# Optimization experiments

Measured on AMD Instinct MI355X. Metric: run time of the kernel, lower is better.

## Reference

```python
import jax, jax.numpy as jnp
import numpy as np

N, E, D_IN, D_AGG, D_OUT = 40000, 640000, 128, 128, 64


def setup_inputs() -> dict:
    key = jax.random.key(0)
    ks = jax.random.split(key, 16)

    def lin(kw, fan_in, fan_out):
        s = 1.0 / np.sqrt(fan_in)
        return jax.random.uniform(kw, (fan_in, fan_out), jnp.float32, -s, s)

    return {
        "x_self": jax.random.normal(ks[0], (N, D_IN), jnp.float32),
        "x_neighbor": jax.random.normal(ks[1], (N, D_AGG), jnp.float32),
        "edge_index": jax.random.randint(ks[2], (2, E), 0, N, jnp.int64),
        # linear_in_self: D_IN -> 2*D_OUT
        "W_in_self": lin(ks[3], D_IN, 2 * D_OUT),
        "b_in_self": jnp.zeros((2 * D_OUT,), jnp.float32),
        # linear_out_self: D_IN + 2*D_OUT -> D_OUT
        "W_out_self": lin(ks[4], D_IN + 2 * D_OUT, D_OUT),
        "b_out_self": jnp.zeros((D_OUT,), jnp.float32),
        # gcn1: D_IN -> 2*D_OUT ; gcn2: 2*D_OUT -> D_OUT
        "Wg1": lin(ks[5], D_IN, 2 * D_OUT),
        "bg1": jnp.zeros((2 * D_OUT,), jnp.float32),
        "Wg2": lin(ks[6], 2 * D_OUT, D_OUT),
        "bg2": jnp.zeros((D_OUT,), jnp.float32),
        # linear_out: D_AGG + D_OUT -> D_OUT
        "W_out": lin(ks[7], D_AGG + D_OUT, D_OUT),
        "b_out": jnp.zeros((D_OUT,), jnp.float32),
    }


def _gcn(x, W, b, row, col, norm, n):
    # PyG GCNConv: linear transform, then normalized gather/scatter-add
    h = x @ W                              # [N, out]
    msg = h[row] * norm[:, None]           # [E+N, out] gathered messages
    return jax.ops.segment_sum(msg, col, num_segments=n) + b


def reference(x_self, x_neighbor, edge_index,
              W_in_self, b_in_self, W_out_self, b_out_self,
              Wg1, bg1, Wg2, bg2, W_out, b_out):
    n = x_self.shape[0]
    loop = jnp.arange(n, dtype=edge_index.dtype)
    row = jnp.concatenate([edge_index[0], loop])   # sources (+ self-loops)
    col = jnp.concatenate([edge_index[1], loop])   # targets (+ self-loops)
    deg = jax.ops.segment_sum(jnp.ones_like(col, jnp.float32), col, num_segments=n)
    dis = jnp.where(deg > 0, jax.lax.rsqrt(jnp.maximum(deg, 1.0)), 0.0)
    norm = dis[row] * dis[col]

    # self branch
    l1 = jax.nn.relu(x_self @ W_in_self + b_in_self)
    l1 = jnp.concatenate([x_self, l1], axis=1)
    l1 = l1 @ W_out_self + b_out_self

    # GCN aggregation branch (no activation between convs, per source)
    g1 = _gcn(x_self, Wg1, bg1, row, col, norm, n)
    g2 = _gcn(g1, Wg2, bg2, row, col, norm, n)
    x2 = jnp.concatenate([x_neighbor, g2], axis=1) @ W_out + b_out
    return (l1, x2)
```

## Files before the change

### kernel.cpp

```cpp
#include <hip/hip_runtime.h>
#include <hip/hip_fp16.h>

typedef short s8v __attribute__((ext_vector_type(8)));
typedef float f4v __attribute__((ext_vector_type(4)));
typedef unsigned short u16x8 __attribute__((ext_vector_type(8)));

__device__ __forceinline__ unsigned short f2bf(float f) {
  unsigned u = __float_as_uint(f);
  u = (u + 0x7fffu + ((u >> 16) & 1u)) >> 16;
  return (unsigned short)u;
}
__device__ __forceinline__ float bf2f(unsigned short s) {
  return __uint_as_float(((unsigned)s) << 16);
}

__device__ __forceinline__ void pack_one(const float* __restrict__ W,
                                         unsigned short* __restrict__ P,
                                         int NCf, int stride, int t) {
  const int lane = t & 63;
  const int ct = (t >> 6) % (NCf / 16);
  const int kc = (t >> 6) / (NCf / 16);
  const int col = ct * 16 + (lane & 15);
  const int krow = kc * 32 + (lane >> 4) * 8;
  unsigned short tmp[8];
#pragma unroll
  for (int j = 0; j < 8; ++j) tmp[j] = f2bf(W[(krow + j) * stride + col]);
  uint4 o;
  o.x = (unsigned)tmp[0] | ((unsigned)tmp[1] << 16);
  o.y = (unsigned)tmp[2] | ((unsigned)tmp[3] << 16);
  o.z = (unsigned)tmp[4] | ((unsigned)tmp[5] << 16);
  o.w = (unsigned)tmp[6] | ((unsigned)tmp[7] << 16);
  reinterpret_cast<uint4*>(P)[t] = o;
}

__global__ __launch_bounds__(256) void prep_kernel(
    const float* __restrict__ x, unsigned short* __restrict__ S1,
    int* __restrict__ deg, const float* __restrict__ Wis,
    const float* __restrict__ Wos, const float* __restrict__ Wo,
    unsigned short* __restrict__ P, int cvtB, int zeroB, int N) {
  const int blk = blockIdx.x;
  const int tid = threadIdx.x;
  if (blk < cvtB) {
    const int i = blk * 256 + tid;
    const float4 v = reinterpret_cast<const float4*>(x)[i];
    ushort4 o;
    o.x = f2bf(v.x); o.y = f2bf(v.y); o.z = f2bf(v.z); o.w = f2bf(v.w);
    reinterpret_cast<ushort4*>(S1)[i] = o;
    return;
  }
  const int b1 = blk - cvtB;
  if (b1 < zeroB) {
    const int i = b1 * 256 + tid;
    if (i < N) deg[i] = 0;
    return;
  }
  const int b = b1 - zeroB;
  if (b < 4)        pack_one(Wis,            P + 0,     64, 128, b * 256 + tid);
  else if (b < 8)   pack_one(Wis + 64,       P + 8192,  64, 128, (b - 4) * 256 + tid);
  else if (b < 12)  pack_one(Wos,            P + 16384, 64, 64,  (b - 8) * 256 + tid);
  else if (b < 16)  pack_one(Wos + 128 * 64, P + 24576, 64, 64,  (b - 12) * 256 + tid);
  else if (b < 20)  pack_one(Wo,             P + 32768, 64, 64,  (b - 16) * 256 + tid);
  else              pack_one(Wo + 128 * 64,  P + 40960, 64, 64,  (b - 20) * 256 + tid);
}

__global__ __launch_bounds__(256) void deg_w12_kernel(
    const int* __restrict__ cols, int* __restrict__ deg, int E, int degB,
    const float* __restrict__ Wg1, const float* __restrict__ Wg2,
    const float* __restrict__ bg1, unsigned short* __restrict__ P12,
    float* __restrict__ bvec) {
  const int blk = blockIdx.x;
  if (blk < degB) {
    const int i = blk * 256 + threadIdx.x;
    if (i < E) atomicAdd(&deg[cols[i]], 1);
    return;
  }
  const int b = blk - degB;
  if (b < 32) {
    const int t = b * 256 + threadIdx.x;
    const int i = t >> 6, j = t & 63;
    float acc = 0.f;
    for (int k = 0; k < 128; ++k)
      acc = fmaf(Wg1[i * 128 + k], Wg2[k * 64 + j], acc);
    const int kc = i >> 5;
    const int lane = ((i >> 3) & 3) * 16 + (j & 15);
    const int jj = i & 7;
    const int ct = j >> 4;
    P12[((kc * 4 + ct) * 64 + lane) * 8 + jj] = f2bf(acc);
  } else if (threadIdx.x < 64) {
    const int j = threadIdx.x;
    float acc = 0.f;
    for (int k = 0; k < 128; ++k) acc = fmaf(bg1[k], Wg2[k * 64 + j], acc);
    bvec[j] = acc;
  }
}

__device__ __forceinline__ void stage16k(unsigned short* __restrict__ Bs,
                                         const unsigned short* __restrict__ src) {
  uint4* d = reinterpret_cast<uint4*>(Bs);
  const uint4* s = reinterpret_cast<const uint4*>(src);
  for (int i = threadIdx.x; i < 1024; i += 256) d[i] = s[i];
}

__device__ __forceinline__ void load_a_bf16(s8v a[4],
                                            const unsigned short* __restrict__ A,
                                            int arow, int koff) {
#pragma unroll
  for (int kc = 0; kc < 4; ++kc)
    a[kc] = *reinterpret_cast<const s8v*>(A + (long long)arow * 128 + kc * 32 + koff);
}

__device__ __forceinline__ void load_a_f32(s8v a[4],
                                           const float* __restrict__ A,
                                           int arow, int koff) {
#pragma unroll
  for (int kc = 0; kc < 4; ++kc) {
    const float4 f0 = *reinterpret_cast<const float4*>(
        A + (long long)arow * 128 + kc * 32 + koff);
    const float4 f1 = *reinterpret_cast<const float4*>(
        A + (long long)arow * 128 + kc * 32 + koff + 4);
    s8v r;
    r[0] = (short)f2bf(f0.x); r[1] = (short)f2bf(f0.y);
    r[2] = (short)f2bf(f0.z); r[3] = (short)f2bf(f0.w);
    r[4] = (short)f2bf(f1.x); r[5] = (short)f2bf(f1.y);
    r[6] = (short)f2bf(f1.z); r[7] = (short)f2bf(f1.w);
    a[kc] = r;
  }
}

__device__ __forceinline__ void mfma_panel(f4v acc[4], const s8v a[4],
                                           const unsigned short* __restrict__ Bs,
                                           int lane) {
#pragma unroll
  for (int kc = 0; kc < 4; ++kc)
#pragma unroll
    for (int ct = 0; ct < 4; ++ct) {
      const s8v b =
          *reinterpret_cast<const s8v*>(&Bs[((kc * 4 + ct) * 64 + lane) * 8]);
      acc[ct] = __builtin_amdgcn_mfma_f32_16x16x32_bf16(a[kc], b, acc[ct], 0, 0, 0);
    }
}

__device__ __forceinline__ void gemm1_body(
    unsigned short* __restrict__ Bs, const unsigned short* __restrict__ S1,
    const unsigned short* __restrict__ P, const float* __restrict__ bis,
    unsigned short* __restrict__ S2h, int blk) {
  const int tid = threadIdx.x;
  const int wave = tid >> 6, lane = tid & 63;
  const int row0 = blk * 64 + wave * 16;
  const int arow = row0 + (lane & 15);
  const int koff = (lane >> 4) * 8;
  s8v a1[4];
  load_a_bf16(a1, S1, arow, koff);
  f4v acc[8] = {};
#pragma unroll
  for (int h = 0; h < 2; ++h) {
    if (h) __syncthreads();
    stage16k(Bs, P + h * 8192);
    __syncthreads();
    mfma_panel(&acc[h * 4], a1, Bs, lane);
  }
  const int crow0 = row0 + (lane >> 4) * 4;
  const int ccol = lane & 15;
#pragma unroll
  for (int h = 0; h < 2; ++h)
#pragma unroll
    for (int ctl = 0; ctl < 4; ++ctl) {
      const int col = h * 64 + ctl * 16 + ccol;
      const float bv = bis[col];
#pragma unroll
      for (int r = 0; r < 4; ++r) {
        const float v = fmaxf(acc[h * 4 + ctl][r] + bv, 0.f);
        S2h[(long long)(crow0 + r) * 128 + col] = f2bf(v);
      }
    }
}

__device__ __forceinline__ void gemm2_body(
    unsigned short* __restrict__ Bs, const unsigned short* __restrict__ S1,
    const unsigned short* __restrict__ S2h, const unsigned short* __restrict__ P0,
    const unsigned short* __restrict__ P1, const float* __restrict__ bos,
    float* __restrict__ out1, int blk) {
  const int tid = threadIdx.x;
  const int wave = tid >> 6, lane = tid & 63;
  const int row0 = blk * 64 + wave * 16;
  const int arow = row0 + (lane & 15);
  const int koff = (lane >> 4) * 8;
  s8v a1[4], a2[4];
  load_a_bf16(a1, S1, arow, koff);
  load_a_bf16(a2, S2h, arow, koff);
  f4v acc[4] = {};
  stage16k(Bs, P0);
  __syncthreads();
  mfma_panel(acc, a1, Bs, lane);
  __syncthreads();
  stage16k(Bs, P1);
  __syncthreads();
  mfma_panel(acc, a2, Bs, lane);
  const int crow0 = row0 + (lane >> 4) * 4;
  const int ccol = lane & 15;
#pragma unroll
  for (int ct = 0; ct < 4; ++ct) {
    const int col = ct * 16 + ccol;
    const float bv = bos[col];
#pragma unroll
    for (int r = 0; r < 4; ++r)
      out1[(long long)(crow0 + r) * 64 + col] = acc[ct][r] + bv;
  }
}

template <int K1, bool OUT_BF16, bool A1F32, bool ACCUM>
__device__ __forceinline__ void gemm64_body(
    unsigned short* __restrict__ Bs, const void* __restrict__ A1v,
    const unsigned short* __restrict__ P1, const float* __restrict__ bias,
    void* __restrict__ Cout, int blk) {
  constexpr int KC1 = K1 / 32;
  const int tid = threadIdx.x;
  {
    uint4* d = reinterpret_cast<uint4*>(Bs);
    const uint4* s = reinterpret_cast<const uint4*>(P1);
    constexpr int n1 = K1 * 64 / 8;
    for (int i = tid; i < n1; i += 256) d[i] = s[i];
  }
  const int wave = tid >> 6, lane = tid & 63;
  const int row0 = blk * 64 + wave * 16;
  const int arow = row0 + (lane & 15);
  const int koff = (lane >> 4) * 8;
  s8v a1[KC1];
  if constexpr (A1F32) {
    const float* A1f = (const float*)A1v;
#pragma unroll
    for (int kc = 0; kc < KC1; ++kc) {
      const float4 f0 = *reinterpret_cast<const float4*>(
          A1f + (long long)arow * K1 + kc * 32 + koff);
      const float4 f1 = *reinterpret_cast<const float4*>(
          A1f + (long long)arow * K1 + kc * 32 + koff + 4);
      s8v r;
      r[0] = (short)f2bf(f0.x); r[1] = (short)f2bf(f0.y);
      r[2] = (short)f2bf(f0.z); r[3] = (short)f2bf(f0.w);
      r[4] = (short)f2bf(f1.x); r[5] = (short)f2bf(f1.y);
      r[6] = (short)f2bf(f1.z); r[7] = (short)f2bf(f1.w);
      a1[kc] = r;
    }
  } else {
    const unsigned short* A1b = (const unsigned short*)A1v;
#pragma unroll
    for (int kc = 0; kc < KC1; ++kc)
      a1[kc] = *reinterpret_cast<const s8v*>(A1b + (long long)arow * K1 +
                                             kc * 32 + koff);
  }
  __syncthreads();
  f4v acc[4] = {};
#pragma unroll
  for (int kc = 0; kc < KC1; ++kc)
#pragma unroll
    for (int ct = 0; ct < 4; ++ct) {
      const s8v b =
          *reinterpret_cast<const s8v*>(&Bs[((kc * 4 + ct) * 64 + lane) * 8]);
      acc[ct] = __builtin_amdgcn_mfma_f32_16x16x32_bf16(a1[kc], b, acc[ct], 0, 0, 0);
    }
  const int crow0 = row0 + (lane >> 4) * 4;
  const int ccol = lane & 15;
#pragma unroll
  for (int ct = 0; ct < 4; ++ct) {
    const int col = ct * 16 + ccol;
    const float bv = bias ? bias[col] : 0.f;
#pragma unroll
    for (int r = 0; r < 4; ++r) {
      const long long idx = (long long)(crow0 + r) * 64 + col;
      float v = acc[ct][r] + bv;
      if (ACCUM) v += ((float*)Cout)[idx];
      if (OUT_BF16)
        ((unsigned short*)Cout)[idx] = f2bf(v);
      else
        ((float*)Cout)[idx] = v;
    }
  }
}

template <bool PASS_B>
__device__ __forceinline__ void gather_body(
    const unsigned short* __restrict__ h, const unsigned* __restrict__ csr,
    const int* __restrict__ off, const float* __restrict__ dis,
    float* __restrict__ s_out, const float* __restrict__ s_in,
    const float* __restrict__ bvec, const float* __restrict__ bias,
    unsigned short* __restrict__ out, int N, int gb, int nblk) {
  const int wid = (gb * 256 + (int)threadIdx.x) >> 6;
  const int lane = threadIdx.x & 63;
  const int grp = lane >> 3;
  const int sl = lane & 7;
  const int stride = nblk * 32;

  float bb[8], bv[8];
  if constexpr (PASS_B) {
    const float4 b0 = *reinterpret_cast<const float4*>(bias + sl * 8);
    const float4 b1 = *reinterpret_cast<const float4*>(bias + sl * 8 + 4);
    bb[0] = b0.x; bb[1] = b0.y; bb[2] = b0.z; bb[3] = b0.w;
    bb[4] = b1.x; bb[5] = b1.y; bb[6] = b1.z; bb[7] = b1.w;
    const float4 v0 = *reinterpret_cast<const float4*>(bvec + sl * 8);
    const float4 v1 = *reinterpret_cast<const float4*>(bvec + sl * 8 + 4);
    bv[0] = v0.x; bv[1] = v0.y; bv[2] = v0.z; bv[3] = v0.w;
    bv[4] = v1.x; bv[5] = v1.y; bv[6] = v1.z; bv[7] = v1.w;
  }

  for (int n = wid * 8 + grp; n < N; n += stride) {
    const float dn = dis[n];
    const float dn2 = dn * dn;
    float a[8];
    {
      const u16x8 hv =
          *reinterpret_cast<const u16x8*>(h + (long long)n * 64 + sl * 8);
#pragma unroll
      for (int q = 0; q < 8; ++q) a[q] = bf2f(hv[q]) * dn2;
    }
    float sw = dn2;
    const int start = (n == 0) ? 0 : off[n - 1];
    const int end = off[n];
    int j = start;
    for (; j + 3 < end; j += 4) {
      const unsigned e0 = csr[j], e1 = csr[j + 1];
      const unsigned e2 = csr[j + 2], e3 = csr[j + 3];
      const u16x8 u0 = *reinterpret_cast<const u16x8*>(
          h + (long long)(e0 & 0xffffu) * 64 + sl * 8);
      const u16x8 u1 = *reinterpret_cast<const u16x8*>(
          h + (long long)(e1 & 0xffffu) * 64 + sl * 8);
      const u16x8 u2 = *reinterpret_cast<const u16x8*>(
          h + (long long)(e2 & 0xffffu) * 64 + sl * 8);
      const u16x8 u3 = *reinterpret_cast<const u16x8*>(
          h + (long long)(e3 & 0xffffu) * 64 + sl * 8);
      const float w0 = __half2float(__ushort_as_half((unsigned short)(e0 >> 16)));
      const float w1 = __half2float(__ushort_as_half((unsigned short)(e1 >> 16)));
      const float w2 = __half2float(__ushort_as_half((unsigned short)(e2 >> 16)));
      const float w3 = __half2float(__ushort_as_half((unsigned short)(e3 >> 16)));
#pragma unroll
      for (int q = 0; q < 8; ++q) {
        a[q] = fmaf(bf2f(u0[q]), w0, a[q]);
        a[q] = fmaf(bf2f(u1[q]), w1, a[q]);
        a[q] = fmaf(bf2f(u2[q]), w2, a[q]);
        a[q] = fmaf(bf2f(u3[q]), w3, a[q]);
      }
      if constexpr (!PASS_B) sw += (w0 + w1) + (w2 + w3);
    }
    for (; j < end; ++j) {
      const unsigned e = csr[j];
      const u16x8 u = *reinterpret_cast<const u16x8*>(
          h + (long long)(e & 0xffffu) * 64 + sl * 8);
      const float w = __half2float(__ushort_as_half((unsigned short)(e >> 16)));
#pragma unroll
      for (int q = 0; q < 8; ++q) a[q] = fmaf(bf2f(u[q]), w, a[q]);
      if constexpr (!PASS_B) sw += w;
    }
    u16x8 o;
    if constexpr (!PASS_B) {
      if (sl == 0) s_out[n] = sw;
#pragma unroll
      for (int q = 0; q < 8; ++q) o[q] = f2bf(a[q]);
    } else {
      const float si = s_in[n];
#pragma unroll
      for (int q = 0; q < 8; ++q) o[q] = f2bf(fmaf(si, bv[q], a[q] + bb[q]));
    }
    *reinterpret_cast<u16x8*>(out + (long long)n * 64 + sl * 8) = o;
  }
}

__global__ __launch_bounds__(1024) void scan1_kernel(
    const int* __restrict__ deg, int* __restrict__ off, int* __restrict__ part,
    float* __restrict__ dis, int N) {
  __shared__ int s[1024];
  const int tid = threadIdx.x;
  const int i = blockIdx.x * 1024 + tid;
  const int v = (i < N) ? deg[i] : 0;
  if (i < N) dis[i] = rsqrtf((float)v + 1.0f);
  s[tid] = v;
  __syncthreads();
  for (int o = 1; o < 1024; o <<= 1) {
    const int t = (tid >= o) ? s[tid - o] : 0;
    __syncthreads();
    s[tid] += t;
    __syncthreads();
  }
  if (i < N) off[i] = s[tid] - v;
  if (tid == 1023) part[blockIdx.x] = s[1023];
}

__global__ __launch_bounds__(1024) void scan3_kernel(
    int* __restrict__ off, const int* __restrict__ part, int N) {
  __shared__ int pp;
  if (threadIdx.x < 64) {
    int v = (threadIdx.x < blockIdx.x) ? part[threadIdx.x] : 0;
#pragma unroll
    for (int o = 32; o > 0; o >>= 1) v += __shfl_down(v, o, 64);
    if (threadIdx.x == 0) pp = v;
  }
  __syncthreads();
  const int i = blockIdx.x * 1024 + threadIdx.x;
  if (i < N) off[i] += pp;
}

__global__ __launch_bounds__(256) void mega_kernel(
    const unsigned short* __restrict__ S1, const float* __restrict__ x_nb,
    const unsigned short* __restrict__ P, const float* __restrict__ bis,
    const float* __restrict__ bo, unsigned short* __restrict__ S2h,
    unsigned short* __restrict__ S4, float* __restrict__ out2,
    const int* __restrict__ rows, const int* __restrict__ cols,
    int* __restrict__ off, const float* __restrict__ dis,
    unsigned* __restrict__ csr, int E, int GB) {
  __shared__ unsigned short Bs[8192];
  const int b = blockIdx.x;
  if (b < GB) {
    gemm1_body(Bs, S1, P, bis, S2h, b);
  } else if (b < 2 * GB) {
    gemm64_body<128, true, false, false>(Bs, S1, P + 45056, nullptr, S4, b - GB);
  } else if (b < 3 * GB) {
    gemm64_body<128, false, true, false>(Bs, x_nb, P + 32768, bo, out2, b - 2 * GB);
  } else {
    const int i = (b - 3 * GB) * 256 + (int)threadIdx.x;
    if (i < E) {
      const int c = cols[i];
      const int r = rows[i];
      const int pos = atomicAdd(&off[c], 1);
      const unsigned wb = __half_as_ushort(__float2half(dis[r] * dis[c]));
      csr[pos] = (wb << 16) | (unsigned)r;
    }
  }
}

__global__ __launch_bounds__(256) void g2ga_kernel(
    const unsigned short* __restrict__ S1, const unsigned short* __restrict__ S2h,
    const unsigned short* __restrict__ P, const float* __restrict__ bos,
    float* __restrict__ out1, const unsigned short* __restrict__ S4,
    const unsigned* __restrict__ csr, const int* __restrict__ off,
    const float* __restrict__ dis, float* __restrict__ s_out,
    unsigned short* __restrict__ S3, int N, int GB, int GGB) {
  __shared__ unsigned short Bs[8192];
  const int b = blockIdx.x;
  if (b < GB) {
    gemm2_body(Bs, S1, S2h, P + 16384, P + 24576, bos, out1, b);
  } else {
    gather_body<false>(S4, csr, off, dis, s_out, nullptr, nullptr, nullptr, S3,
                       N, b - GB, GGB);
  }
}

__global__ __launch_bounds__(256) void gatherB_kernel(
    const unsigned short* __restrict__ S3, const unsigned* __restrict__ csr,
    const int* __restrict__ off, const float* __restrict__ dis,
    const float* __restrict__ s_in, const float* __restrict__ bvec,
    const float* __restrict__ bias, unsigned short* __restrict__ G2, int N) {
  gather_body<true>(S3, csr, off, dis, nullptr, s_in, bvec, bias, G2, N,
                    blockIdx.x, gridDim.x);
}

__global__ __launch_bounds__(256) void g4b_kernel(
    const unsigned short* __restrict__ G2, const unsigned short* __restrict__ P,
    float* __restrict__ out2) {
  __shared__ unsigned short Bs[4096];
  gemm64_body<64, false, false, true>(Bs, G2, P + 40960, nullptr, out2,
                                      blockIdx.x);
}

extern "C" void kernel_launch(void* const* d_in, const int* in_sizes, int n_in,
                              void* d_out, int out_size, void* d_ws,
                              size_t ws_size, hipStream_t stream) {
  const float* x_self = (const float*)d_in[0];
  const float* x_nb = (const float*)d_in[1];
  const int* ei = (const int*)d_in[2];
  const float* Wis = (const float*)d_in[3];
  const float* bis = (const float*)d_in[4];
  const float* Wos = (const float*)d_in[5];
  const float* bos = (const float*)d_in[6];
  const float* Wg1 = (const float*)d_in[7];
  const float* bg1 = (const float*)d_in[8];
  const float* Wg2 = (const float*)d_in[9];
  const float* bg2 = (const float*)d_in[10];
  const float* Wo = (const float*)d_in[11];
  const float* bo = (const float*)d_in[12];

  const int N = in_sizes[0] / 128;
  const int E = (int)(in_sizes[2] / 2);
  const int* rows = ei;
  const int* cols = ei + E;

  float* out1 = (float*)d_out;
  float* out2 = out1 + (long long)N * 64;

  float* dis = (float*)d_ws;
  int* deg = (int*)(dis + N);
  int* off = deg + N;
  int* part = off + N + 16;
  float* s = (float*)(part + 64);
  float* bvec = s + N;
  unsigned* csr = (unsigned*)(bvec + 64);
  unsigned short* S1 = (unsigned short*)(csr + E);
  unsigned short* S2h = S1 + (long long)N * 128;
  unsigned short* S3 = S2h + (long long)N * 128;
  unsigned short* S4 = S3 + (long long)N * 64;
  unsigned short* P = S4 + (long long)N * 64;
  unsigned short* pW12 = P + 45056;

  const int NB = (N + 1023) / 1024;
  const int GB = N / 64;
  const int GGB = (N + 31) / 32;

  const int cvtB = (N * 32 + 255) / 256;
  const int zeroB = (N + 255) / 256;
  const int degB = (E + 255) / 256;

  prep_kernel<<<cvtB + zeroB + 22, 256, 0, stream>>>(
      x_self, S1, deg, Wis, Wos, Wo, P, cvtB, zeroB, N);
  deg_w12_kernel<<<degB + 33, 256, 0, stream>>>(cols, deg, E, degB, Wg1, Wg2,
                                                bg1, pW12, bvec);
  scan1_kernel<<<NB, 1024, 0, stream>>>(deg, off, part, dis, N);
  scan3_kernel<<<NB, 1024, 0, stream>>>(off, part, N);
  mega_kernel<<<3 * GB + degB, 256, 0, stream>>>(
      S1, x_nb, P, bis, bo, S2h, S4, out2, rows, cols, off, dis, csr, E, GB);
  g2ga_kernel<<<GB + GGB, 256, 0, stream>>>(S1, S2h, P, bos, out1, S4, csr,
                                            off, dis, s, S3, N, GB, GGB);
  gatherB_kernel<<<GGB, 256, 0, stream>>>(S3, csr, off, dis, s, bvec, bg2, S1, N);
  g4b_kernel<<<GB, 256, 0, stream>>>(S1, P, out2);
}
```

Baseline: 130.3 us.

## Fuse final 64x64 output GEMM into second gather and reorder block dispatch

The separate g4b GEMM kernel is removed: the second GCN gather now multiplies each aggregated 64-wide row by the W_out slice held in shared memory (fp32, using lane shuffles) and accumulates into out2 directly. This drops one launch and a bf16 round trip of the G2 intermediate. In exchange, the gather kernel does per-row scalar FMA work in place of MFMA. Block ordering in mega_kernel and g2ga_kernel is also swapped so the CSR-fill and gather blocks are dispatched before the GEMM blocks, which should help the latency-bound work start early.

```diff
diff --git a/kernel.cpp b/kernel.cpp
--- a/kernel.cpp
+++ b/kernel.cpp
@@ -59,8 +59,7 @@
   else if (b < 8)   pack_one(Wis + 64,       P + 8192,  64, 128, (b - 4) * 256 + tid);
   else if (b < 12)  pack_one(Wos,            P + 16384, 64, 64,  (b - 8) * 256 + tid);
   else if (b < 16)  pack_one(Wos + 128 * 64, P + 24576, 64, 64,  (b - 12) * 256 + tid);
-  else if (b < 20)  pack_one(Wo,             P + 32768, 64, 64,  (b - 16) * 256 + tid);
-  else              pack_one(Wo + 128 * 64,  P + 40960, 64, 64,  (b - 20) * 256 + tid);
+  else              pack_one(Wo,             P + 32768, 64, 64,  (b - 16) * 256 + tid);
 }
 
 __global__ __launch_bounds__(256) void deg_w12_kernel(
@@ -109,24 +108,6 @@
     a[kc] = *reinterpret_cast<const s8v*>(A + (long long)arow * 128 + kc * 32 + koff);
 }
 
-__device__ __forceinline__ void load_a_f32(s8v a[4],
-                                           const float* __restrict__ A,
-                                           int arow, int koff) {
-#pragma unroll
-  for (int kc = 0; kc < 4; ++kc) {
-    const float4 f0 = *reinterpret_cast<const float4*>(
-        A + (long long)arow * 128 + kc * 32 + koff);
-    const float4 f1 = *reinterpret_cast<const float4*>(
-        A + (long long)arow * 128 + kc * 32 + koff + 4);
-    s8v r;
-    r[0] = (short)f2bf(f0.x); r[1] = (short)f2bf(f0.y);
-    r[2] = (short)f2bf(f0.z); r[3] = (short)f2bf(f0.w);
-    r[4] = (short)f2bf(f1.x); r[5] = (short)f2bf(f1.y);
-    r[6] = (short)f2bf(f1.z); r[7] = (short)f2bf(f1.w);
-    a[kc] = r;
-  }
-}
-
 __device__ __forceinline__ void mfma_panel(f4v acc[4], const s8v a[4],
                                            const unsigned short* __restrict__ Bs,
                                            int lane) {
@@ -208,32 +189,30 @@
   }
 }
 
-template <int K1, bool OUT_BF16, bool A1F32, bool ACCUM>
+template <bool OUT_BF16, bool A1F32>
 __device__ __forceinline__ void gemm64_body(
     unsigned short* __restrict__ Bs, const void* __restrict__ A1v,
     const unsigned short* __restrict__ P1, const float* __restrict__ bias,
     void* __restrict__ Cout, int blk) {
-  constexpr int KC1 = K1 / 32;
   const int tid = threadIdx.x;
   {
     uint4* d = reinterpret_cast<uint4*>(Bs);
     const uint4* s = reinterpret_cast<const uint4*>(P1);
-    constexpr int n1 = K1 * 64 / 8;
-    for (int i = tid; i < n1; i += 256) d[i] = s[i];
+    for (int i = tid; i < 1024; i += 256) d[i] = s[i];
   }
   const int wave = tid >> 6, lane = tid & 63;
   const int row0 = blk * 64 + wave * 16;
   const int arow = row0 + (lane & 15);
   const int koff = (lane >> 4) * 8;
-  s8v a1[KC1];
+  s8v a1[4];
   if constexpr (A1F32) {
     const float* A1f = (const float*)A1v;
 #pragma unroll
-    for (int kc = 0; kc < KC1; ++kc) {
+    for (int kc = 0; kc < 4; ++kc) {
       const float4 f0 = *reinterpret_cast<const float4*>(
-          A1f + (long long)arow * K1 + kc * 32 + koff);
+          A1f + (long long)arow * 128 + kc * 32 + koff);
       const float4 f1 = *reinterpret_cast<const float4*>(
-          A1f + (long long)arow * K1 + kc * 32 + koff + 4);
+          A1f + (long long)arow * 128 + kc * 32 + koff + 4);
       s8v r;
       r[0] = (short)f2bf(f0.x); r[1] = (short)f2bf(f0.y);
       r[2] = (short)f2bf(f0.z); r[3] = (short)f2bf(f0.w);
@@ -242,22 +221,11 @@
       a1[kc] = r;
     }
   } else {
-    const unsigned short* A1b = (const unsigned short*)A1v;
-#pragma unroll
-    for (int kc = 0; kc < KC1; ++kc)
-      a1[kc] = *reinterpret_cast<const s8v*>(A1b + (long long)arow * K1 +
-                                             kc * 32 + koff);
+    load_a_bf16(a1, (const unsigned short*)A1v, arow, koff);
   }
   __syncthreads();
   f4v acc[4] = {};
-#pragma unroll
-  for (int kc = 0; kc < KC1; ++kc)
-#pragma unroll
-    for (int ct = 0; ct < 4; ++ct) {
-      const s8v b =
-          *reinterpret_cast<const s8v*>(&Bs[((kc * 4 + ct) * 64 + lane) * 8]);
-      acc[ct] = __builtin_amdgcn_mfma_f32_16x16x32_bf16(a1[kc], b, acc[ct], 0, 0, 0);
-    }
+  mfma_panel(acc, a1, Bs, lane);
   const int crow0 = row0 + (lane >> 4) * 4;
   const int ccol = lane & 15;
 #pragma unroll
@@ -268,7 +236,6 @@
     for (int r = 0; r < 4; ++r) {
       const long long idx = (long long)(crow0 + r) * 64 + col;
       float v = acc[ct][r] + bv;
-      if (ACCUM) v += ((float*)Cout)[idx];
       if (OUT_BF16)
         ((unsigned short*)Cout)[idx] = f2bf(v);
       else
@@ -277,30 +244,16 @@
   }
 }
 
-template <bool PASS_B>
-__device__ __forceinline__ void gather_body(
+__device__ __forceinline__ void gatherA_body(
     const unsigned short* __restrict__ h, const unsigned* __restrict__ csr,
     const int* __restrict__ off, const float* __restrict__ dis,
-    float* __restrict__ s_out, const float* __restrict__ s_in,
-    const float* __restrict__ bvec, const float* __restrict__ bias,
-    unsigned short* __restrict__ out, int N, int gb, int nblk) {
+    float* __restrict__ s_out, unsigned short* __restrict__ out, int N,
+    int gb, int nblk) {
   const int wid = (gb * 256 + (int)threadIdx.x) >> 6;
   const int lane = threadIdx.x & 63;
   const int grp = lane >> 3;
   const int sl = lane & 7;
   const int stride = nblk * 32;
-
-  float bb[8], bv[8];
-  if constexpr (PASS_B) {
-    const float4 b0 = *reinterpret_cast<const float4*>(bias + sl * 8);
-    const float4 b1 = *reinterpret_cast<const float4*>(bias + sl * 8 + 4);
-    bb[0] = b0.x; bb[1] = b0.y; bb[2] = b0.z; bb[3] = b0.w;
-    bb[4] = b1.x; bb[5] = b1.y; bb[6] = b1.z; bb[7] = b1.w;
-    const float4 v0 = *reinterpret_cast<const float4*>(bvec + sl * 8);
-    const float4 v1 = *reinterpret_cast<const float4*>(bvec + sl * 8 + 4);
-    bv[0] = v0.x; bv[1] = v0.y; bv[2] = v0.z; bv[3] = v0.w;
-    bv[4] = v1.x; bv[5] = v1.y; bv[6] = v1.z; bv[7] = v1.w;
-  }
 
   for (int n = wid * 8 + grp; n < N; n += stride) {
     const float dn = dis[n];
@@ -338,7 +291,7 @@
         a[q] = fmaf(bf2f(u2[q]), w2, a[q]);
         a[q] = fmaf(bf2f(u3[q]), w3, a[q]);
       }
-      if constexpr (!PASS_B) sw += (w0 + w1) + (w2 + w3);
+      sw += (w0 + w1) + (w2 + w3);
     }
     for (; j < end; ++j) {
       const unsigned e = csr[j];
@@ -347,18 +300,12 @@
       const float w = __half2float(__ushort_as_half((unsigned short)(e >> 16)));
 #pragma unroll
       for (int q = 0; q < 8; ++q) a[q] = fmaf(bf2f(u[q]), w, a[q]);
-      if constexpr (!PASS_B) sw += w;
-    }
+      sw += w;
+    }
+    if (sl == 0) s_out[n] = sw;
     u16x8 o;
-    if constexpr (!PASS_B) {
-      if (sl == 0) s_out[n] = sw;
-#pragma unroll
-      for (int q = 0; q < 8; ++q) o[q] = f2bf(a[q]);
-    } else {
-      const float si = s_in[n];
-#pragma unroll
-      for (int q = 0; q < 8; ++q) o[q] = f2bf(fmaf(si, bv[q], a[q] + bb[q]));
-    }
+#pragma unroll
+    for (int q = 0; q < 8; ++q) o[q] = f2bf(a[q]);
     *reinterpret_cast<u16x8*>(out + (long long)n * 64 + sl * 8) = o;
   }
 }
@@ -404,17 +351,11 @@
     unsigned short* __restrict__ S4, float* __restrict__ out2,
     const int* __restrict__ rows, const int* __restrict__ cols,
     int* __restrict__ off, const float* __restrict__ dis,
-    unsigned* __restrict__ csr, int E, int GB) {
+    unsigned* __restrict__ csr, int E, int degB, int GB) {
   __shared__ unsigned short Bs[8192];
   const int b = blockIdx.x;
-  if (b < GB) {
-    gemm1_body(Bs, S1, P, bis, S2h, b);
-  } else if (b < 2 * GB) {
-    gemm64_body<128, true, false, false>(Bs, S1, P + 45056, nullptr, S4, b - GB);
-  } else if (b < 3 * GB) {
-    gemm64_body<128, false, true, false>(Bs, x_nb, P + 32768, bo, out2, b - 2 * GB);
-  } else {
-    const int i = (b - 3 * GB) * 256 + (int)threadIdx.x;
+  if (b < degB) {
+    const int i = b * 256 + (int)threadIdx.x;
     if (i < E) {
       const int c = cols[i];
       const int r = rows[i];
@@ -422,6 +363,12 @@
       const unsigned wb = __half_as_ushort(__float2half(dis[r] * dis[c]));
       csr[pos] = (wb << 16) | (unsigned)r;
     }
+  } else if (b < degB + GB) {
+    gemm1_body(Bs, S1, P, bis, S2h, b - degB);
+  } else if (b < degB + 2 * GB) {
+    gemm64_body<true, false>(Bs, S1, P + 45056, nullptr, S4, b - degB - GB);
+  } else {
+    gemm64_body<false, true>(Bs, x_nb, P + 32768, bo, out2, b - degB - 2 * GB);
   }
 }
 
@@ -434,11 +381,10 @@
     unsigned short* __restrict__ S3, int N, int GB, int GGB) {
   __shared__ unsigned short Bs[8192];
   const int b = blockIdx.x;
-  if (b < GB) {
-    gemm2_body(Bs, S1, S2h, P + 16384, P + 24576, bos, out1, b);
+  if (b < GGB) {
+    gatherA_body(S4, csr, off, dis, s_out, S3, N, b, GGB);
   } else {
-    gather_body<false>(S4, csr, off, dis, s_out, nullptr, nullptr, nullptr, S3,
-                       N, b - GB, GGB);
+    gemm2_body(Bs, S1, S2h, P + 16384, P + 24576, bos, out1, b - GGB);
   }
 }
 
@@ -446,17 +392,104 @@
     const unsigned short* __restrict__ S3, const unsigned* __restrict__ csr,
     const int* __restrict__ off, const float* __restrict__ dis,
     const float* __restrict__ s_in, const float* __restrict__ bvec,
-    const float* __restrict__ bias, unsigned short* __restrict__ G2, int N) {
-  gather_body<true>(S3, csr, off, dis, nullptr, s_in, bvec, bias, G2, N,
-                    blockIdx.x, gridDim.x);
-}
-
-__global__ __launch_bounds__(256) void g4b_kernel(
-    const unsigned short* __restrict__ G2, const unsigned short* __restrict__ P,
-    float* __restrict__ out2) {
-  __shared__ unsigned short Bs[4096];
-  gemm64_body<64, false, false, true>(Bs, G2, P + 40960, nullptr, out2,
-                                      blockIdx.x);
+    const float* __restrict__ bias, const float* __restrict__ Wo1,
+    float* __restrict__ out2, int N) {
+  __shared__ float Ws[4096];
+  for (int i = threadIdx.x; i < 1024; i += 256)
+    reinterpret_cast<float4*>(Ws)[i] = reinterpret_cast<const float4*>(Wo1)[i];
+  __syncthreads();
+
+  const int wid = (blockIdx.x * 256 + (int)threadIdx.x) >> 6;
+  const int lane = threadIdx.x & 63;
+  const int grp = lane >> 3;
+  const int sl = lane & 7;
+  const int base = lane & 56;
+  const int stride = gridDim.x * 32;
+
+  float bb[8], bv[8];
+  {
+    const float4 b0 = *reinterpret_cast<const float4*>(bias + sl * 8);
+    const float4 b1 = *reinterpret_cast<const float4*>(bias + sl * 8 + 4);
+    bb[0] = b0.x; bb[1] = b0.y; bb[2] = b0.z; bb[3] = b0.w;
+    bb[4] = b1.x; bb[5] = b1.y; bb[6] = b1.z; bb[7] = b1.w;
+    const float4 v0 = *reinterpret_cast<const float4*>(bvec + sl * 8);
+    const float4 v1 = *reinterpret_cast<const float4*>(bvec + sl * 8 + 4);
+    bv[0] = v0.x; bv[1] = v0.y; bv[2] = v0.z; bv[3] = v0.w;
+    bv[4] = v1.x; bv[5] = v1.y; bv[6] = v1.z; bv[7] = v1.w;
+  }
+
+  for (int n = wid * 8 + grp; n < N; n += stride) {
+    const float dn = dis[n];
+    const float dn2 = dn * dn;
+    float a[8];
+    {
+      const u16x8 hv =
+          *reinterpret_cast<const u16x8*>(S3 + (long long)n * 64 + sl * 8);
+#pragma unroll
+      for (int q = 0; q < 8; ++q) a[q] = bf2f(hv[q]) * dn2;
+    }
+    const int start = (n == 0) ? 0 : off[n - 1];
+    const int end = off[n];
+    int j = start;
+    for (; j + 3 < end; j += 4) {
+      const unsigned e0 = csr[j], e1 = csr[j + 1];
+      const unsigned e2 = csr[j + 2], e3 = csr[j + 3];
+      const u16x8 u0 = *reinterpret_cast<const u16x8*>(
+          S3 + (long long)(e0 & 0xffffu) * 64 + sl * 8);
+      const u16x8 u1 = *reinterpret_cast<const u16x8*>(
+          S3 + (long long)(e1 & 0xffffu) * 64 + sl * 8);
+      const u16x8 u2 = *reinterpret_cast<const u16x8*>(
+          S3 + (long long)(e2 & 0xffffu) * 64 + sl * 8);
+      const u16x8 u3 = *reinterpret_cast<const u16x8*>(
+          S3 + (long long)(e3 & 0xffffu) * 64 + sl * 8);
+      const float w0 = __half2float(__ushort_as_half((unsigned short)(e0 >> 16)));
+      const float w1 = __half2float(__ushort_as_half((unsigned short)(e1 >> 16)));
+      const float w2 = __half2float(__ushort_as_half((unsigned short)(e2 >> 16)));
+      const float w3 = __half2float(__ushort_as_half((unsigned short)(e3 >> 16)));
+#pragma unroll
+      for (int q = 0; q < 8; ++q) {
+        a[q] = fmaf(bf2f(u0[q]), w0, a[q]);
+        a[q] = fmaf(bf2f(u1[q]), w1, a[q]);
+        a[q] = fmaf(bf2f(u2[q]), w2, a[q]);
+        a[q] = fmaf(bf2f(u3[q]), w3, a[q]);
+      }
+    }
+    for (; j < end; ++j) {
+      const unsigned e = csr[j];
+      const u16x8 u = *reinterpret_cast<const u16x8*>(
+          S3 + (long long)(e & 0xffffu) * 64 + sl * 8);
+      const float w = __half2float(__ushort_as_half((unsigned short)(e >> 16)));
+#pragma unroll
+      for (int q = 0; q < 8; ++q) a[q] = fmaf(bf2f(u[q]), w, a[q]);
+    }
+    const float si = s_in[n];
+#pragma unroll
+    for (int q = 0; q < 8; ++q) a[q] = fmaf(si, bv[q], a[q] + bb[q]);
+
+    float oa[8] = {};
+#pragma unroll
+    for (int q = 0; q < 8; ++q) {
+#pragma unroll
+      for (int t = 0; t < 8; ++t) {
+        const float gv = __shfl(a[t], base + q);
+        const int k = q * 8 + t;
+        const float4 w0 = *reinterpret_cast<const float4*>(&Ws[k * 64 + sl * 8]);
+        const float4 w1 =
+            *reinterpret_cast<const float4*>(&Ws[k * 64 + sl * 8 + 4]);
+        oa[0] = fmaf(gv, w0.x, oa[0]); oa[1] = fmaf(gv, w0.y, oa[1]);
+        oa[2] = fmaf(gv, w0.z, oa[2]); oa[3] = fmaf(gv, w0.w, oa[3]);
+        oa[4] = fmaf(gv, w1.x, oa[4]); oa[5] = fmaf(gv, w1.y, oa[5]);
+        oa[6] = fmaf(gv, w1.z, oa[6]); oa[7] = fmaf(gv, w1.w, oa[7]);
+      }
+    }
+    float* op = out2 + (long long)n * 64 + sl * 8;
+    float4 c0 = *reinterpret_cast<float4*>(op);
+    float4 c1 = *reinterpret_cast<float4*>(op + 4);
+    c0.x += oa[0]; c0.y += oa[1]; c0.z += oa[2]; c0.w += oa[3];
+    c1.x += oa[4]; c1.y += oa[5]; c1.z += oa[6]; c1.w += oa[7];
+    *reinterpret_cast<float4*>(op) = c0;
+    *reinterpret_cast<float4*>(op + 4) = c1;
+  }
 }
 
 extern "C" void kernel_launch(void* const* d_in, const int* in_sizes, int n_in,
@@ -506,16 +539,17 @@
   const int zeroB = (N + 255) / 256;
   const int degB = (E + 255) / 256;
 
-  prep_kernel<<<cvtB + zeroB + 22, 256, 0, stream>>>(
+  prep_kernel<<<cvtB + zeroB + 20, 256, 0, stream>>>(
       x_self, S1, deg, Wis, Wos, Wo, P, cvtB, zeroB, N);
   deg_w12_kernel<<<degB + 33, 256, 0, stream>>>(cols, deg, E, degB, Wg1, Wg2,
                                                 bg1, pW12, bvec);
   scan1_kernel<<<NB, 1024, 0, stream>>>(deg, off, part, dis, N);
   scan3_kernel<<<NB, 1024, 0, stream>>>(off, part, N);
-  mega_kernel<<<3 * GB + degB, 256, 0, stream>>>(
-      S1, x_nb, P, bis, bo, S2h, S4, out2, rows, cols, off, dis, csr, E, GB);
-  g2ga_kernel<<<GB + GGB, 256, 0, stream>>>(S1, S2h, P, bos, out1, S4, csr,
+  mega_kernel<<<degB + 3 * GB, 256, 0, stream>>>(
+      S1, x_nb, P, bis, bo, S2h, S4, out2, rows, cols, off, dis, csr, E, degB,
+      GB);
+  g2ga_kernel<<<GGB + GB, 256, 0, stream>>>(S1, S2h, P, bos, out1, S4, csr,
                                             off, dis, s, S3, N, GB, GGB);
-  gatherB_kernel<<<GGB, 256, 0, stream>>>(S3, csr, off, dis, s, bvec, bg2, S1, N);
-  g4b_kernel<<<GB, 256, 0, stream>>>(S1, P, out2);
-}
+  gatherB_kernel<<<GGB, 256, 0, stream>>>(S3, csr, off, dis, s, bvec, bg2,
+                                          Wo + 128 * 64, out2, N);
+}
```

New measurement: 197.6 us. 51.7% more time.
